# Kernel tuning notes

Hardware: AMD Instinct MI355X
Metric: run time of the kernel (lower is better)

## Reference

```python
import jax, jax.numpy as jnp
import numpy as np

NUM_ENT = 40000
NUM_REL = 100
EMBED_DIM = 256
FEAT_DIM = 768
BATCH = 32
SEQ_LEN = 3
MASK_POS = 2
EPS = 1e-12


def setup_inputs() -> dict:
    key = jax.random.key(0)
    k1, k2, k3, k4 = jax.random.split(key, 4)
    ent_pkl = jax.random.normal(k1, (NUM_ENT, FEAT_DIM), dtype=jnp.float32)
    other_emb = jax.random.normal(k2, (NUM_ENT + NUM_REL + 3 - NUM_ENT, EMBED_DIM), dtype=jnp.float32)
    proj_W = jax.random.normal(k3, (EMBED_DIM, FEAT_DIM), dtype=jnp.float32) * (1.0 / np.sqrt(FEAT_DIM))
    batch_input_ids = jax.random.randint(k4, (BATCH, SEQ_LEN), 0, NUM_ENT + NUM_REL + 3, dtype=jnp.int64)
    return {
        "ent_pkl": ent_pkl,
        "other_emb": other_emb,
        "proj_W": proj_W,
        "batch_input_ids": batch_input_ids,
        "batch_mask_position": MASK_POS,
    }


def reference(ent_pkl, other_emb, proj_W, batch_input_ids, batch_mask_position):
    # unity embeddings: [other[0], proj(ent_pkl), other[1:]] -> [num_ent+num_rel+3, d]
    ent_proj = ent_pkl @ proj_W.T  # Linear(feat_dim, embed_dim, bias=False)
    unity = jnp.concatenate([other_emb[:1], ent_proj, other_emb[1:]], axis=0)

    mp = int(batch_mask_position)
    # drop the masked slot, keep up to 3 tokens total -> [B, 2]
    query_input = jnp.concatenate(
        [batch_input_ids[:, :mp], batch_input_ids[:, mp + 1:3]], axis=1)
    query_emb = unity[query_input]  # [B, 2, d]
    # F.normalize(dim=-1): x / max(||x||_2, eps)
    norm = jnp.sqrt(jnp.sum(query_emb * query_emb, axis=-1, keepdims=True))
    query_emb = query_emb / jnp.maximum(norm, EPS)
    query_sum = jnp.sum(query_emb, axis=1)  # [B, d]

    E_embed = unity[:NUM_ENT + 1]  # [num_ent+1, d]
    # broadcast L1 distance: [B, num_ent+1]
    score = -jnp.sum(jnp.abs(query_sum[:, None, :] - E_embed[None, :, :]), axis=-1)
    return score
```

## Files before the change

kernel.cpp:

```cpp
#include <hip/hip_runtime.h>
#include <hip/hip_bf16.h>
#include <stdint.h>

#define NE 40000
#define FD 768
#define ED 256
#define NB 32
#define OUTC (NE + 1)

typedef __bf16 bf16x8 __attribute__((ext_vector_type(8)));
typedef float f32x4 __attribute__((ext_vector_type(4)));
typedef float f32x16 __attribute__((ext_vector_type(16)));
typedef _Float16 f16x2 __attribute__((ext_vector_type(2)));
typedef _Float16 f16x4 __attribute__((ext_vector_type(4)));

#define WS_QS 0
#define WS_N01 (32 * 1024)
#define WS_WB (96 * 1024)

__device__ __forceinline__ f16x2 pabs2(f16x2 d) {
    union { f16x2 h; unsigned u; } v; v.h = d; v.u &= 0x7FFF7FFFu; return v.h;
}

__device__ __forceinline__ bf16x8 cvt8(f32x4 lo, f32x4 hi) {
    bf16x8 v;
    v[0] = (__bf16)lo[0]; v[1] = (__bf16)lo[1]; v[2] = (__bf16)lo[2]; v[3] = (__bf16)lo[3];
    v[4] = (__bf16)hi[0]; v[5] = (__bf16)hi[1]; v[6] = (__bf16)hi[2]; v[7] = (__bf16)hi[3];
    return v;
}

__device__ __forceinline__ void gload16(const void* g, void* l) {
    __builtin_amdgcn_global_load_lds(
        (const __attribute__((address_space(1))) unsigned int*)g,
        (__attribute__((address_space(3))) unsigned int*)l, 16, 0, 0);
}


__global__ __launch_bounds__(512) void prep_kernel(
    const float* __restrict__ ent_pkl, const float* __restrict__ W,
    const int* __restrict__ ids, const int* __restrict__ mpos,
    __bf16* __restrict__ Wf, float* __restrict__ n01_raw)
{
    __shared__ __align__(16) unsigned char smem[65536];
    const int t = threadIdx.x;

    if (blockIdx.x < 96) {
        const int i = blockIdx.x * 2048 + t * 4;
        const int r = i / FD, c = i - r * FD;
        float4 v = *(const float4*)(W + i);
        __bf16 o[4] = {(__bf16)v.x, (__bf16)v.y, (__bf16)v.z, (__bf16)v.w};
        const int f = ((r >> 5) * 48 + (c >> 4)) * 64 + (r & 31) + ((c >> 3) & 1) * 32;
        *(ushort4*)(Wf + (size_t)f * 8 + (c & 7)) = *(const ushort4*)o;
        return;
    }

    const int l = t & 63;
    const int w = t >> 6;
    const int m31 = l & 31;
    const int dh = l >> 5;
    const int sw = m31 & 15;
    const int mp = mpos[0];
    const bool wide = (ids[1] == 0 && ids[3] == 0 && ids[5] == 0);

    const int r1 = t >> 4;
    const int goff = ((t & 15) ^ (r1 & 15)) * 4;
    int rowA, rowB;
    {
        int s = r1;
        int b = s >> 1, sq = s & 1;
        int col = (sq < mp) ? sq : sq + 1;
        int flat = b * 3 + col;
        int idx = wide ? ids[flat * 2] : ids[flat];
        rowA = (idx >= 1 && idx <= NE) ? idx - 1 : 0;
        s = r1 + 32;
        b = s >> 1; sq = s & 1;
        col = (sq < mp) ? sq : sq + 1;
        flat = b * 3 + col;
        idx = wide ? ids[flat * 2] : ids[flat];
        rowB = (idx >= 1 && idx <= NE) ? idx - 1 : 0;
    }
    const float* ab1 = ent_pkl + (size_t)rowA * FD + goff;
    const float* ab2 = ent_pkl + (size_t)rowB * FD + goff;
    const float* Wr = W + (size_t)(32 * w + m31) * FD + 8 * dh;

    f32x16 acc0, acc1;
#pragma unroll
    for (int i = 0; i < 16; ++i) { acc0[i] = 0.f; acc1[i] = 0.f; }

#define P_ISSUE(P) { char* lb = (char*)smem + ((P) & 3) * 16384 + t * 16; \
        gload16(ab1 + (P) * 64, lb); gload16(ab2 + (P) * 64, lb + 8192); }

#define P_PHASE(P, NW, DOISS) \
    asm volatile("s_waitcnt vmcnt(" #NW ")" ::: "memory"); \
    __builtin_amdgcn_s_barrier(); \
    __builtin_amdgcn_sched_barrier(0); \
    { \
        f32x4 wv[8]; \
        _Pragma("unroll") for (int c2 = 0; c2 < 4; ++c2) { \
            wv[2 * c2]     = *(const f32x4*)(Wr + 16 * (4 * (P) + c2)); \
            wv[2 * c2 + 1] = *(const f32x4*)(Wr + 16 * (4 * (P) + c2) + 4); \
        } \
        __builtin_amdgcn_sched_barrier(0); \
        if (DOISS) P_ISSUE((P) + 3); \
        const char* Ab = (const char*)smem + ((P) & 3) * 16384; \
        _Pragma("unroll") for (int c2 = 0; c2 < 4; ++c2) { \
            const int u0 = (4 * c2 + 2 * dh) ^ sw; \
            const char* pa = Ab + (m31 * 16 + u0) * 16; \
            const char* pb = Ab + (m31 * 16 + (u0 ^ 1)) * 16; \
            f32x4 lo0 = *(const f32x4*)pa,          hi0 = *(const f32x4*)pb; \
            f32x4 lo1 = *(const f32x4*)(pa + 8192), hi1 = *(const f32x4*)(pb + 8192); \
            bf16x8 bv = cvt8(wv[2 * c2], wv[2 * c2 + 1]); \
            acc0 = __builtin_amdgcn_mfma_f32_32x32x16_bf16(cvt8(lo0, hi0), bv, acc0, 0, 0, 0); \
            acc1 = __builtin_amdgcn_mfma_f32_32x32x16_bf16(cvt8(lo1, hi1), bv, acc1, 0, 0, 0); \
        } \
    }

    P_ISSUE(0); P_ISSUE(1); P_ISSUE(2);
    P_PHASE(0, 4, 1)  P_PHASE(1, 8, 1)  P_PHASE(2, 8, 1)  P_PHASE(3, 8, 1)
    P_PHASE(4, 8, 1)  P_PHASE(5, 8, 1)  P_PHASE(6, 8, 1)  P_PHASE(7, 8, 1)
    P_PHASE(8, 8, 1)  P_PHASE(9, 8, 0)  P_PHASE(10, 8, 0) P_PHASE(11, 8, 0)

#pragma unroll
    for (int r = 0; r < 16; ++r) {
        const int erow = (r & 3) + 8 * (r >> 2) + 4 * dh;
        n01_raw[erow * ED + 32 * w + m31] = acc0[r];
        n01_raw[(32 + erow) * ED + 32 * w + m31] = acc1[r];
    }
}

__global__ __launch_bounds__(256) void qsum_kernel(
    const float* __restrict__ other_emb, const float* __restrict__ n01_raw,
    const int* __restrict__ ids, const int* __restrict__ mpos,
    _Float16* __restrict__ qh, float* __restrict__ out)
{
    __shared__ float red[4];
    __shared__ float nshare;
    const int b = blockIdx.x, t = threadIdx.x;
    const int mp = mpos[0];
    const bool wide = (ids[1] == 0 && ids[3] == 0 && ids[5] == 0);

    float q = 0.f;
#pragma unroll
    for (int s = 0; s < 2; ++s) {
        const int col = (s < mp) ? s : s + 1;
        const int flat = b * 3 + col;
        const int idx = wide ? ids[flat * 2] : ids[flat];
        float v;
        if (idx >= 1 && idx <= NE) v = n01_raw[(b * 2 + s) * ED + t];
        else if (idx == 0) v = other_emb[t];
        else v = other_emb[(size_t)(idx - NE) * ED + t];

        float ss = v * v;
#pragma unroll
        for (int o = 32; o > 0; o >>= 1) ss += __shfl_down(ss, o, 64);
        if ((t & 63) == 0) red[t >> 6] = ss;
        __syncthreads();
        if (t == 0) nshare = fmaxf(sqrtf(red[0] + red[1] + red[2] + red[3]), 1e-12f);
        __syncthreads();
        q += v / nshare;
        __syncthreads();
    }
    qh[b * ED + t] = (_Float16)q;

    float d = fabsf(q - other_emb[t]);
#pragma unroll
    for (int o = 32; o > 0; o >>= 1) d += __shfl_down(d, o, 64);
    if ((t & 63) == 0) red[t >> 6] = d;
    __syncthreads();
    if (t == 0) out[(size_t)b * OUTC] = -(red[0] + red[1] + red[2] + red[3]);
}

#define SP 256

__global__ __launch_bounds__(512, 4) void gemm_score_kernel(
    const float* __restrict__ ent_pkl, const __bf16* __restrict__ Wf,
    const _Float16* __restrict__ qh, float* __restrict__ out)
{
    __shared__ __align__(16) unsigned char smem[65536];
    _Float16* Sb = (_Float16*)smem;
    _Float16* qL = (_Float16*)(smem + 32768);

    const int t = threadIdx.x;
    const int l = t & 63;
    const int w = t >> 6;
    const int m31 = l & 31;
    const int dh = l >> 5;
    const int sw = m31 & 15;
    const int e0 = blockIdx.x * 64;

    f32x16 acc0, acc1;
#pragma unroll
    for (int i = 0; i < 16; ++i) { acc0[i] = 0.f; acc1[i] = 0.f; }

    const int r1 = t >> 4;
    const int goff = ((t & 15) ^ (r1 & 15)) * 4;
    const float* ab1 = ent_pkl + (size_t)(e0 + r1) * FD + goff;
    const float* ab2 = ent_pkl + (size_t)(e0 + r1 + 32) * FD + goff;
    const __bf16* bp = Wf + (size_t)w * 24576 + (size_t)l * 8;

    bf16x8 bvA[4], bvB[4];

#define G_ISSUE(P) { char* lb = (char*)smem + ((P) & 3) * 16384 + t * 16; \
        gload16(ab1 + (P) * 64, lb); gload16(ab2 + (P) * 64, lb + 8192); }

#define G_PHASE(P, NW, BUSE, BNEXT, DOISS, DOLOAD) \
    asm volatile("s_waitcnt vmcnt(" #NW ")" ::: "memory"); \
    __builtin_amdgcn_s_barrier(); \
    __builtin_amdgcn_sched_barrier(0); \
    if (DOLOAD) { _Pragma("unroll") for (int c2 = 0; c2 < 4; ++c2) \
        BNEXT[c2] = *(const bf16x8*)(bp + (size_t)(4 * ((P) + 1) + c2) * 512); } \
    __builtin_amdgcn_sched_barrier(0); \
    if (DOISS) G_ISSUE((P) + 3); \
    { \
        const char* Ab = (const char*)smem + ((P) & 3) * 16384; \
        _Pragma("unroll") for (int c2 = 0; c2 < 4; ++c2) { \
            const int u0 = (4 * c2 + 2 * dh) ^ sw; \
            const char* pa = Ab + (m31 * 16 + u0) * 16; \
            const char* pb = Ab + (m31 * 16 + (u0 ^ 1)) * 16; \
            f32x4 lo0 = *(const f32x4*)pa,          hi0 = *(const f32x4*)pb; \
            f32x4 lo1 = *(const f32x4*)(pa + 8192), hi1 = *(const f32x4*)(pb + 8192); \
            acc0 = __builtin_amdgcn_mfma_f32_32x32x16_bf16(cvt8(lo0, hi0), BUSE[c2], acc0, 0, 0, 0); \
            acc1 = __builtin_amdgcn_mfma_f32_32x32x16_bf16(cvt8(lo1, hi1), BUSE[c2], acc1, 0, 0, 0); \
        } \
    }

    G_ISSUE(0); G_ISSUE(1); G_ISSUE(2);
#pragma unroll
    for (int c2 = 0; c2 < 4; ++c2) bvA[c2] = *(const bf16x8*)(bp + (size_t)c2 * 512);

    G_PHASE(0, 8, bvA, bvB, 1, 1)   G_PHASE(1, 8, bvB, bvA, 1, 1)
    G_PHASE(2, 8, bvA, bvB, 1, 1)   G_PHASE(3, 8, bvB, bvA, 1, 1)
    G_PHASE(4, 8, bvA, bvB, 1, 1)   G_PHASE(5, 8, bvB, bvA, 1, 1)
    G_PHASE(6, 8, bvA, bvB, 1, 1)   G_PHASE(7, 8, bvB, bvA, 1, 1)
    G_PHASE(8, 8, bvA, bvB, 1, 1)   G_PHASE(9, 8, bvB, bvA, 0, 1)
    G_PHASE(10, 6, bvA, bvB, 0, 1)  G_PHASE(11, 4, bvB, bvA, 0, 0)

    __syncthreads();
    const int colg = 8 * w + (m31 >> 2);
    const int csub = m31 & 3;
#pragma unroll
    for (int r = 0; r < 16; ++r) {
        const int erow = (r & 3) + 8 * (r >> 2) + 4 * dh;
        const int ph = (((colg ^ (erow & 15)) << 2) | csub);
        Sb[erow * SP + ph] = (_Float16)acc0[r];
        Sb[(32 + erow) * SP + ph] = (_Float16)acc1[r];
    }
    {
        const uint4* qsrc = (const uint4*)qh;
        uint4* qdst = (uint4*)qL;
        qdst[t] = qsrc[t];
        qdst[t + 512] = qsrc[t + 512];
    }
    __syncthreads();

    const int wu = __builtin_amdgcn_readfirstlane(w);
    const f16x4* q0 = (const f16x4*)(qL + (size_t)(4 * wu + 0) * ED);
    const f16x4* q1 = (const f16x4*)(qL + (size_t)(4 * wu + 1) * ED);
    const f16x4* q2 = (const f16x4*)(qL + (size_t)(4 * wu + 2) * ED);
    const f16x4* q3 = (const f16x4*)(qL + (size_t)(4 * wu + 3) * ED);
    const int swl = l & 15;
    const _Float16* xbase = Sb + (size_t)l * SP;

    float s0 = 0.f, s1 = 0.f, s2 = 0.f, s3 = 0.f;
    for (int cb = 0; cb < 8; ++cb) {
        f16x2 t0 = {0, 0}, t1 = {0, 0}, t2 = {0, 0}, t3 = {0, 0};
#pragma unroll
        for (int ci = 0; ci < 8; ++ci) {
            const int c = cb * 8 + ci;
            f16x4 xv = *(const f16x4*)(xbase + ((c ^ swl) << 2));
            f16x2 xlo = __builtin_shufflevector(xv, xv, 0, 1);
            f16x2 xhi = __builtin_shufflevector(xv, xv, 2, 3);
            f16x4 qa = q0[c], qb = q1[c], qc = q2[c], qd = q3[c];
            t0 = t0 + pabs2(__builtin_shufflevector(qa, qa, 0, 1) - xlo);
            t0 = t0 + pabs2(__builtin_shufflevector(qa, qa, 2, 3) - xhi);
            t1 = t1 + pabs2(__builtin_shufflevector(qb, qb, 0, 1) - xlo);
            t1 = t1 + pabs2(__builtin_shufflevector(qb, qb, 2, 3) - xhi);
            t2 = t2 + pabs2(__builtin_shufflevector(qc, qc, 0, 1) - xlo);
            t2 = t2 + pabs2(__builtin_shufflevector(qc, qc, 2, 3) - xhi);
            t3 = t3 + pabs2(__builtin_shufflevector(qd, qd, 0, 1) - xlo);
            t3 = t3 + pabs2(__builtin_shufflevector(qd, qd, 2, 3) - xhi);
        }
        s0 += (float)t0[0] + (float)t0[1];
        s1 += (float)t1[0] + (float)t1[1];
        s2 += (float)t2[0] + (float)t2[1];
        s3 += (float)t3[0] + (float)t3[1];
    }
    float* ob = out + 1 + e0 + l;
    __builtin_nontemporal_store(-s0, ob + (size_t)(4 * wu + 0) * OUTC);
    __builtin_nontemporal_store(-s1, ob + (size_t)(4 * wu + 1) * OUTC);
    __builtin_nontemporal_store(-s2, ob + (size_t)(4 * wu + 2) * OUTC);
    __builtin_nontemporal_store(-s3, ob + (size_t)(4 * wu + 3) * OUTC);
}

extern "C" void kernel_launch(void* const* d_in, const int* in_sizes, int n_in,
                              void* d_out, int out_size, void* d_ws, size_t ws_size,
                              hipStream_t stream) {
    const float* ent_pkl = (const float*)d_in[0];
    const float* other_emb = (const float*)d_in[1];
    const float* proj_W = (const float*)d_in[2];
    const int* ids = (const int*)d_in[3];
    const int* mpos = (const int*)d_in[4];
    float* out = (float*)d_out;

    _Float16* qh = (_Float16*)((char*)d_ws + WS_QS);
    float* n01_raw = (float*)((char*)d_ws + WS_N01);
    __bf16* Wf = (__bf16*)((char*)d_ws + WS_WB);

    prep_kernel<<<97, 512, 0, stream>>>(ent_pkl, proj_W, ids, mpos, Wf, n01_raw);
    qsum_kernel<<<NB, 256, 0, stream>>>(other_emb, n01_raw, ids, mpos, qh, out);
    gemm_score_kernel<<<NE / 64, 512, 0, stream>>>(ent_pkl, Wf, qh, out);
}
```

Before: 267.2 us.

## Fold query-sum into prep kernel and restage GEMM A tiles via registers as bf16

Merges the query normalisation and sum step into the last block of the prep kernel, using shared memory and sub-wave shuffles, which removes one kernel launch and a global round trip for the projected query rows. The GEMM kernel stops copying fp32 A tiles straight to LDS with async loads. Instead it loads them into registers, converts them to bf16 and double-buffers them in LDS, which cuts LDS to 48KB and moves conversion out of the MFMA loop. Each block starts at a different K phase (blockIdx&3) to spread memory traffic. The trade-off is less latency hiding, since the async multi-stage prefetch is replaced by a register-staged scheme with a barrier every phase.

Result: faster. 237.5 us (-11.1%).

```diff
diff --git a/kernel.cpp b/kernel.cpp
--- a/kernel.cpp
+++ b/kernel.cpp
@@ -15,7 +15,6 @@
 typedef _Float16 f16x4 __attribute__((ext_vector_type(4)));
 
 #define WS_QS 0
-#define WS_N01 (32 * 1024)
 #define WS_WB (96 * 1024)
 
 __device__ __forceinline__ f16x2 pabs2(f16x2 d) {
@@ -35,11 +34,11 @@
         (__attribute__((address_space(3))) unsigned int*)l, 16, 0, 0);
 }
 
-
 __global__ __launch_bounds__(512) void prep_kernel(
     const float* __restrict__ ent_pkl, const float* __restrict__ W,
+    const float* __restrict__ other_emb,
     const int* __restrict__ ids, const int* __restrict__ mpos,
-    __bf16* __restrict__ Wf, float* __restrict__ n01_raw)
+    __bf16* __restrict__ Wf, _Float16* __restrict__ qh, float* __restrict__ out)
 {
     __shared__ __align__(16) unsigned char smem[65536];
     const int t = threadIdx.x;
@@ -120,54 +119,60 @@
     P_PHASE(4, 8, 1)  P_PHASE(5, 8, 1)  P_PHASE(6, 8, 1)  P_PHASE(7, 8, 1)
     P_PHASE(8, 8, 1)  P_PHASE(9, 8, 0)  P_PHASE(10, 8, 0) P_PHASE(11, 8, 0)
 
+    float* n01 = (float*)smem;
+    __syncthreads();
 #pragma unroll
     for (int r = 0; r < 16; ++r) {
         const int erow = (r & 3) + 8 * (r >> 2) + 4 * dh;
-        n01_raw[erow * ED + 32 * w + m31] = acc0[r];
-        n01_raw[(32 + erow) * ED + 32 * w + m31] = acc1[r];
-    }
-}
-
-__global__ __launch_bounds__(256) void qsum_kernel(
-    const float* __restrict__ other_emb, const float* __restrict__ n01_raw,
-    const int* __restrict__ ids, const int* __restrict__ mpos,
-    _Float16* __restrict__ qh, float* __restrict__ out)
-{
-    __shared__ float red[4];
-    __shared__ float nshare;
-    const int b = blockIdx.x, t = threadIdx.x;
-    const int mp = mpos[0];
-    const bool wide = (ids[1] == 0 && ids[3] == 0 && ids[5] == 0);
-
-    float q = 0.f;
-#pragma unroll
-    for (int s = 0; s < 2; ++s) {
-        const int col = (s < mp) ? s : s + 1;
+        n01[erow * ED + 32 * w + m31] = acc0[r];
+        n01[(32 + erow) * ED + 32 * w + m31] = acc1[r];
+    }
+    __syncthreads();
+
+    {
+        const int slot = t >> 3, k = t & 7;
+        const int b = slot >> 1, sq = slot & 1;
+        const int col = (sq < mp) ? sq : sq + 1;
         const int flat = b * 3 + col;
         const int idx = wide ? ids[flat * 2] : ids[flat];
-        float v;
-        if (idx >= 1 && idx <= NE) v = n01_raw[(b * 2 + s) * ED + t];
-        else if (idx == 0) v = other_emb[t];
-        else v = other_emb[(size_t)(idx - NE) * ED + t];
-
-        float ss = v * v;
-#pragma unroll
-        for (int o = 32; o > 0; o >>= 1) ss += __shfl_down(ss, o, 64);
-        if ((t & 63) == 0) red[t >> 6] = ss;
-        __syncthreads();
-        if (t == 0) nshare = fmaxf(sqrtf(red[0] + red[1] + red[2] + red[3]), 1e-12f);
-        __syncthreads();
-        q += v / nshare;
-        __syncthreads();
-    }
-    qh[b * ED + t] = (_Float16)q;
-
-    float d = fabsf(q - other_emb[t]);
-#pragma unroll
-    for (int o = 32; o > 0; o >>= 1) d += __shfl_down(d, o, 64);
-    if ((t & 63) == 0) red[t >> 6] = d;
-    __syncthreads();
-    if (t == 0) out[(size_t)b * OUTC] = -(red[0] + red[1] + red[2] + red[3]);
+        if (!(idx >= 1 && idx <= NE)) {
+            const float* src = (idx == 0) ? other_emb
+                                          : other_emb + (size_t)(idx - NE) * ED;
+            for (int d = k * 32; d < k * 32 + 32; ++d) n01[slot * ED + d] = src[d];
+        }
+    }
+    __syncthreads();
+
+    {
+        const int slot = t >> 3, k = t & 7;
+        float ss = 0.f;
+        const f32x4* v4 = (const f32x4*)(n01 + slot * ED + k * 32);
+#pragma unroll
+        for (int i = 0; i < 8; ++i) {
+            f32x4 v = v4[i];
+            ss += v[0] * v[0] + v[1] * v[1] + v[2] * v[2] + v[3] * v[3];
+        }
+#pragma unroll
+        for (int o = 4; o > 0; o >>= 1) ss += __shfl_xor(ss, o, 8);
+        const float mynorm = fmaxf(sqrtf(ss), 1e-12f);
+        const float otnorm = __shfl_xor(mynorm, 8, 16);
+        const float n0 = (t & 8) ? otnorm : mynorm;
+        const float n1 = (t & 8) ? mynorm : otnorm;
+        const float i0 = 1.f / n0, i1 = 1.f / n1;
+
+        const int b = t >> 4, dt = t & 15;
+        float part = 0.f;
+#pragma unroll
+        for (int i = 0; i < 16; ++i) {
+            const int d = dt * 16 + i;
+            float q = n01[(2 * b) * ED + d] * i0 + n01[(2 * b + 1) * ED + d] * i1;
+            qh[b * ED + d] = (_Float16)q;
+            part += fabsf(q - other_emb[d]);
+        }
+#pragma unroll
+        for (int o = 8; o > 0; o >>= 1) part += __shfl_down(part, o, 16);
+        if (dt == 0) out[(size_t)b * OUTC] = -part;
+    }
 }
 
 #define SP 256
@@ -176,7 +181,9 @@
     const float* __restrict__ ent_pkl, const __bf16* __restrict__ Wf,
     const _Float16* __restrict__ qh, float* __restrict__ out)
 {
-    __shared__ __align__(16) unsigned char smem[65536];
+    __shared__ __align__(16) unsigned char smem[49152];
+    __bf16* A0 = (__bf16*)smem;
+    __bf16* A1 = (__bf16*)(smem + 24576);
     _Float16* Sb = (_Float16*)smem;
     _Float16* qL = (_Float16*)(smem + 32768);
 
@@ -185,55 +192,63 @@
     const int w = t >> 6;
     const int m31 = l & 31;
     const int dh = l >> 5;
-    const int sw = m31 & 15;
     const int e0 = blockIdx.x * 64;
+    const int ph0 = blockIdx.x & 3;
 
     f32x16 acc0, acc1;
 #pragma unroll
     for (int i = 0; i < 16; ++i) { acc0[i] = 0.f; acc1[i] = 0.f; }
 
-    const int r1 = t >> 4;
-    const int goff = ((t & 15) ^ (r1 & 15)) * 4;
-    const float* ab1 = ent_pkl + (size_t)(e0 + r1) * FD + goff;
-    const float* ab2 = ent_pkl + (size_t)(e0 + r1 + 32) * FD + goff;
+    const int srow = t >> 3, sseg = t & 7;
+    const float* abase = ent_pkl + (size_t)(e0 + srow) * FD + sseg * 24;
+    int woff[3];
+#pragma unroll
+    for (int j = 0; j < 3; ++j) {
+        const int uidx = sseg * 3 + j;
+        woff[j] = (uidx * 64 + srow) * 16;
+    }
+
     const __bf16* bp = Wf + (size_t)w * 24576 + (size_t)l * 8;
 
-    bf16x8 bvA[4], bvB[4];
-
-#define G_ISSUE(P) { char* lb = (char*)smem + ((P) & 3) * 16384 + t * 16; \
-        gload16(ab1 + (P) * 64, lb); gload16(ab2 + (P) * 64, lb + 8192); }
-
-#define G_PHASE(P, NW, BUSE, BNEXT, DOISS, DOLOAD) \
-    asm volatile("s_waitcnt vmcnt(" #NW ")" ::: "memory"); \
-    __builtin_amdgcn_s_barrier(); \
-    __builtin_amdgcn_sched_barrier(0); \
-    if (DOLOAD) { _Pragma("unroll") for (int c2 = 0; c2 < 4; ++c2) \
-        BNEXT[c2] = *(const bf16x8*)(bp + (size_t)(4 * ((P) + 1) + c2) * 512); } \
-    __builtin_amdgcn_sched_barrier(0); \
-    if (DOISS) G_ISSUE((P) + 3); \
-    { \
-        const char* Ab = (const char*)smem + ((P) & 3) * 16384; \
-        _Pragma("unroll") for (int c2 = 0; c2 < 4; ++c2) { \
-            const int u0 = (4 * c2 + 2 * dh) ^ sw; \
-            const char* pa = Ab + (m31 * 16 + u0) * 16; \
-            const char* pb = Ab + (m31 * 16 + (u0 ^ 1)) * 16; \
-            f32x4 lo0 = *(const f32x4*)pa,          hi0 = *(const f32x4*)pb; \
-            f32x4 lo1 = *(const f32x4*)(pa + 8192), hi1 = *(const f32x4*)(pb + 8192); \
-            acc0 = __builtin_amdgcn_mfma_f32_32x32x16_bf16(cvt8(lo0, hi0), BUSE[c2], acc0, 0, 0, 0); \
-            acc1 = __builtin_amdgcn_mfma_f32_32x32x16_bf16(cvt8(lo1, hi1), BUSE[c2], acc1, 0, 0, 0); \
-        } \
-    }
-
-    G_ISSUE(0); G_ISSUE(1); G_ISSUE(2);
-#pragma unroll
-    for (int c2 = 0; c2 < 4; ++c2) bvA[c2] = *(const bf16x8*)(bp + (size_t)c2 * 512);
-
-    G_PHASE(0, 8, bvA, bvB, 1, 1)   G_PHASE(1, 8, bvB, bvA, 1, 1)
-    G_PHASE(2, 8, bvA, bvB, 1, 1)   G_PHASE(3, 8, bvB, bvA, 1, 1)
-    G_PHASE(4, 8, bvA, bvB, 1, 1)   G_PHASE(5, 8, bvB, bvA, 1, 1)
-    G_PHASE(6, 8, bvA, bvB, 1, 1)   G_PHASE(7, 8, bvB, bvA, 1, 1)
-    G_PHASE(8, 8, bvA, bvB, 1, 1)   G_PHASE(9, 8, bvB, bvA, 0, 1)
-    G_PHASE(10, 6, bvA, bvB, 0, 1)  G_PHASE(11, 4, bvB, bvA, 0, 0)
+    f32x4 st[6];
+    {
+        const float* ap = abase + ph0 * 192;
+#pragma unroll
+        for (int j = 0; j < 6; ++j) st[j] = *(const f32x4*)(ap + 4 * j);
+#pragma unroll
+        for (int j = 0; j < 3; ++j)
+            *(bf16x8*)((char*)A0 + woff[j]) = cvt8(st[2 * j], st[2 * j + 1]);
+        __syncthreads();
+    }
+
+#pragma unroll
+    for (int p = 0; p < 4; ++p) {
+        const __bf16* Ab = (p & 1) ? A1 : A0;
+        __bf16* An = (p & 1) ? A0 : A1;
+        const int kp = (p + ph0) & 3;
+        const float* np = abase + (size_t)(((p + 1 + ph0) & 3)) * 192;
+        const __bf16* bq = bp + (size_t)kp * 12 * 512;
+#pragma unroll
+        for (int c = 0; c < 12; ++c) {
+            if (p < 3 && (c & 1) == 0) {
+                st[c >> 1] = *(const f32x4*)(np + 4 * (c >> 1));
+                __builtin_amdgcn_sched_barrier(0);
+            }
+            bf16x8 bv = *(const bf16x8*)(bq + (size_t)c * 512);
+            const int u0 = 2 * c + dh;
+            const char* pa = (const char*)Ab + (u0 * 64 + m31) * 16;
+            bf16x8 a0 = *(const bf16x8*)pa;
+            bf16x8 a1 = *(const bf16x8*)(pa + 512);
+            acc0 = __builtin_amdgcn_mfma_f32_32x32x16_bf16(a0, bv, acc0, 0, 0, 0);
+            acc1 = __builtin_amdgcn_mfma_f32_32x32x16_bf16(a1, bv, acc1, 0, 0, 0);
+        }
+        if (p < 3) {
+#pragma unroll
+            for (int j = 0; j < 3; ++j)
+                *(bf16x8*)((char*)An + woff[j]) = cvt8(st[2 * j], st[2 * j + 1]);
+            __syncthreads();
+        }
+    }
 
     __syncthreads();
     const int colg = 8 * w + (m31 >> 2);
@@ -303,10 +318,8 @@
     float* out = (float*)d_out;
 
     _Float16* qh = (_Float16*)((char*)d_ws + WS_QS);
-    float* n01_raw = (float*)((char*)d_ws + WS_N01);
     __bf16* Wf = (__bf16*)((char*)d_ws + WS_WB);
 
-    prep_kernel<<<97, 512, 0, stream>>>(ent_pkl, proj_W, ids, mpos, Wf, n01_raw);
-    qsum_kernel<<<NB, 256, 0, stream>>>(other_emb, n01_raw, ids, mpos, qh, out);
+    prep_kernel<<<97, 512, 0, stream>>>(ent_pkl, proj_W, other_emb, ids, mpos, Wf, qh, out);
     gemm_score_kernel<<<NE / 64, 512, 0, stream>>>(ent_pkl, Wf, qh, out);
 }
```
